# Performance work log

Hardware: AMD Instinct MI355X
Metric: run time of the kernel (lower is better)

The kernel has to match this reference:

```python
import jax, jax.numpy as jnp
import numpy as np

SIZE = 1024      # codebook entries
CODE_DIM = 256   # embedding dim


def setup_inputs() -> dict:
    key = jax.random.key(0)
    k_z, k_w = jax.random.split(key)
    z = jax.random.normal(k_z, (8, CODE_DIM, 16, 32, 32), dtype=jnp.float32)
    # init.uniform_(weight, -1/size, 1/size)
    codebook = jax.random.uniform(
        k_w, (SIZE, CODE_DIM), dtype=jnp.float32,
        minval=-1.0 / SIZE, maxval=1.0 / SIZE)
    return {"z": z, "codebook": codebook}


def reference(z, codebook):
    bs, d, t, h, w = z.shape
    # tokens: [N, d] with N = bs*t*h*w (matches permute(0,2,3,4,1).reshape(-1,d))
    zf = jnp.transpose(z, (0, 2, 3, 4, 1)).reshape(-1, d)
    # squared-distance expansion instead of materializing [size, N, d]:
    # ||z - e||^2 = ||z||^2 - 2 z.e + ||e||^2 ; argmin identical to argmin of norm
    d2 = (jnp.sum(zf * zf, axis=1, keepdims=True)
          - 2.0 * (zf @ codebook.T)
          + jnp.sum(codebook * codebook, axis=1))  # [N, size]
    encoding_indices = jnp.argmin(d2, axis=-1).reshape(bs, t, h, w)
    # gather + permute back to [bs, d, t, h, w]
    quantized = jnp.transpose(codebook[encoding_indices], (0, 4, 1, 2, 3))
    st = z + jax.lax.stop_gradient(quantized - z)  # straight-through output
    return (quantized, st, encoding_indices)
```

## Files before the change

### kernel.cpp

```cpp
#include <hip/hip_runtime.h>
#include <stdint.h>


constexpr int Dd  = 256;
constexpr int SPB = 16384;
constexpr int Nn  = 131072;
constexpr int Kk  = 1024;
constexpr int CCAP = 16;
#define WWIN 2.2e-3f

typedef short short8 __attribute__((ext_vector_type(8)));
typedef float v4f    __attribute__((ext_vector_type(4)));

__device__ __forceinline__ unsigned bf16pk(float a, float b){
  unsigned ua = __float_as_uint(a), ub = __float_as_uint(b);
  ua = (ua + 0x7fffu + ((ua >> 16) & 1u)) >> 16;
  ub = (ub + 0x7fffu + ((ub >> 16) & 1u)) & 0xffff0000u;
  return ua | ub;
}
__device__ __forceinline__ short8 frg(uint4 u){
  union { uint4 a; short8 b; } x; x.a = u; return x.b;
}
__device__ __forceinline__ v4f mfma16(short8 a, short8 b, v4f c){
  return __builtin_amdgcn_mfma_f32_16x16x32_bf16(a, b, c, 0, 0, 0);
}
__device__ __forceinline__ void dma16(const void* g, void* l){
  __builtin_amdgcn_global_load_lds((const __attribute__((address_space(1))) void*)g,
                                   (__attribute__((address_space(3))) void*)l, 16, 0, 0);
}

__global__ __launch_bounds__(64) void cnorm_k(const float* __restrict__ cb,
                                              float* __restrict__ cn){
  const int k = blockIdx.x, l = threadIdx.x;
  const float* row = cb + (size_t)k * Dd;
  float s = 0.f;
  #pragma unroll
  for (int c = 0; c < Dd; c += 64){ float v = row[c + l]; s += v * v; }
  #pragma unroll
  for (int off = 32; off > 0; off >>= 1) s += __shfl_down(s, off, 64);
  if (l == 0) cn[k] = s;
}

__global__ __launch_bounds__(256) void cconv_k(const float* __restrict__ cb,
                                               uint4* __restrict__ Bg){
  const int cc = blockIdx.x, n = threadIdx.x;
  const float* row = cb + (size_t)(cc * 256 + n) * Dd;
  for (int dc = 0; dc < 8; dc++){
    float v[32];
    const float4* rp = (const float4*)(row + dc * 32);
    #pragma unroll
    for (int q = 0; q < 8; q++){
      float4 f = rp[q]; v[4*q]=f.x; v[4*q+1]=f.y; v[4*q+2]=f.z; v[4*q+3]=f.w;
    }
    unsigned hv[16];
    #pragma unroll
    for (int p = 0; p < 16; p++) hv[p] = bf16pk(v[2*p], v[2*p+1]);
    size_t base = ((size_t)cc * 8 + dc) * 1024;
    #pragma unroll
    for (int kq = 0; kq < 4; kq++)
      Bg[base + (size_t)kq*256 + n] = make_uint4(hv[4*kq],hv[4*kq+1],hv[4*kq+2],hv[4*kq+3]);
  }
}

__global__ __launch_bounds__(256) void zconv_k(const float* __restrict__ z,
                                               uint4* __restrict__ Ag){
  const int tid = threadIdx.x, blk = blockIdx.x;
  const int b = blk >> 7, sb = (blk & 127) * 128;
  const int m = tid & 127, kqh = tid >> 7;
  const float* zb = z + (size_t)b * Dd * SPB + sb + m;
  for (int dc = 0; dc < 8; dc++){
    float v[16];
    #pragma unroll
    for (int s = 0; s < 16; s++) v[s] = zb[(size_t)(dc*32 + kqh*16 + s) * SPB];
    unsigned hv[8];
    #pragma unroll
    for (int p = 0; p < 8; p++) hv[p] = bf16pk(v[2*p], v[2*p+1]);
    size_t base = ((size_t)blk * 8 + dc) * 512;
    Ag[base + (size_t)(kqh*2+0)*128 + m] = make_uint4(hv[0],hv[1],hv[2],hv[3]);
    Ag[base + (size_t)(kqh*2+1)*128 + m] = make_uint4(hv[4],hv[5],hv[6],hv[7]);
  }
}

__global__ __launch_bounds__(512) void vq_sweep_k(const uint4* __restrict__ Ag,
                                                  const uint4* __restrict__ Bg,
                                                  const float* __restrict__ cnG,
                                                  int* __restrict__ cntW,
                                                  unsigned short* __restrict__ candW,
                                                  int* __restrict__ abestW){
  __shared__ uint4 AswF[2][2048];
  __shared__ uint4 BswF[2][2048];
  __shared__ unsigned bestP[256];
  __shared__ int cnt[256];
  __shared__ uint4 candU[256][2];
  unsigned short* cand = (unsigned short*)candU;

  const int tid = threadIdx.x, bId = blockIdx.x;
  const int w = tid >> 6, ln = tid & 63;
  const int li = ln & 15, lq = ln >> 4;
  const int wm = w >> 2, wn = w & 3;

  if (tid < 256){ bestP[tid] = 0xFFFFFFFFu; cnt[tid] = 0; }

  float cnr[4][4];
  #pragma unroll
  for (int cc = 0; cc < 4; cc++)
    #pragma unroll
    for (int ni = 0; ni < 4; ni++)
      cnr[cc][ni] = cnG[cc*256 + wn*64 + ni*16 + li];

  int aOff[4], bOff[4];
  #pragma unroll
  for (int c = 0; c < 4; c++){
    const int f = c*512 + w*64 + ln;
    const int dcL = f >> 10, kq = (f >> 8) & 3, mn = f & 255;
    aOff[c] = ((2*bId + (mn >> 7))*8 + dcL)*512 + kq*128 + (mn & 127);
    bOff[c] = dcL*1024 + kq*256 + mn;
  }

  #pragma unroll
  for (int c = 0; c < 4; c++) dma16(Ag + aOff[c], &AswF[0][c*512 + w*64]);
  #pragma unroll
  for (int c = 0; c < 4; c++) dma16(Bg + bOff[c], &BswF[0][c*512 + w*64]);

  v4f acc[8][4];
  #pragma unroll
  for (int cc = 0; cc < 4; cc++){
    const v4f vz = {0.f, 0.f, 0.f, 0.f};
    #pragma unroll
    for (int mi = 0; mi < 8; mi++)
      #pragma unroll
      for (int ni = 0; ni < 4; ni++) acc[mi][ni] = vz;

    #pragma unroll
    for (int ksq = 0; ksq < 4; ksq++){
      const int ks = cc*4 + ksq;
      if (ks < 15){
        const int ksn = ks + 1, bufn = ksn & 1, kqn = ksn & 3;
        #pragma unroll
        for (int c = 0; c < 4; c++)
          dma16(Ag + aOff[c] + kqn*1024, &AswF[bufn][c*512 + w*64]);
        #pragma unroll
        for (int c = 0; c < 4; c++)
          dma16(Bg + bOff[c] + ksn*2048, &BswF[bufn][c*512 + w*64]);
        asm volatile("s_waitcnt vmcnt(8)" ::: "memory");
      } else {
        asm volatile("s_waitcnt vmcnt(0)" ::: "memory");
      }
      __builtin_amdgcn_s_barrier();
      asm volatile("" ::: "memory");

      const int buf = ks & 1;
      #pragma unroll
      for (int dcL = 0; dcL < 2; dcL++){
        const uint4* Ab = &AswF[buf][dcL*1024 + lq*256 + wm*128 + li];
        const uint4* Bb = &BswF[buf][dcL*1024 + lq*256 + wn*64  + li];
        uint4 b0 = Bb[0], b1 = Bb[16], b2 = Bb[32], b3 = Bb[48];
        __builtin_amdgcn_s_setprio(1);
        #pragma unroll
        for (int mi = 0; mi < 8; mi++){
          uint4 av = Ab[mi*16];
          acc[mi][0] = mfma16(frg(av), frg(b0), acc[mi][0]);
          acc[mi][1] = mfma16(frg(av), frg(b1), acc[mi][1]);
          acc[mi][2] = mfma16(frg(av), frg(b2), acc[mi][2]);
          acc[mi][3] = mfma16(frg(av), frg(b3), acc[mi][3]);
        }
        __builtin_amdgcn_s_setprio(0);
      }
      asm volatile("s_waitcnt lgkmcnt(0)" ::: "memory");
      __builtin_amdgcn_s_barrier();
      asm volatile("" ::: "memory");
    }

    const int codeB = cc*256 + wn*64 + li;
    #pragma unroll
    for (int mi = 0; mi < 8; mi++){
      #pragma unroll
      for (int r = 0; r < 4; r++){
        unsigned pm = 0xFFFFFFFFu;
        #pragma unroll
        for (int ni = 0; ni < 4; ni++){
          float s = fmaf(acc[mi][ni][r], -2.0f, cnr[cc][ni]);
          unsigned u = __float_as_uint(s);
          u ^= (unsigned)((int)u >> 31) | 0x80000000u;
          unsigned p = (u & 0xFFFFFC00u) | (unsigned)(codeB + ni*16);
          acc[mi][ni][r] = __uint_as_float(p);
          pm = (pm < p) ? pm : p;
        }
        #pragma unroll
        for (int off = 1; off < 16; off <<= 1){
          unsigned o = (unsigned)__shfl_xor((int)pm, off, 16);
          pm = (pm < o) ? pm : o;
        }
        if (li == 0) atomicMin(&bestP[wm*128 + mi*16 + lq*4 + r], pm);
      }
    }
    asm volatile("s_waitcnt lgkmcnt(0)" ::: "memory");
    __builtin_amdgcn_s_barrier();
    asm volatile("" ::: "memory");
    #pragma unroll
    for (int mi = 0; mi < 8; mi++){
      #pragma unroll
      for (int r = 0; r < 4; r++){
        const int row = wm*128 + mi*16 + lq*4 + r;
        unsigned bp = bestP[row] & 0xFFFFFC00u;
        unsigned fb = (bp & 0x80000000u) ? (bp ^ 0x80000000u) : ~bp;
        float thr = __uint_as_float(fb) + WWIN;
        unsigned tu = __float_as_uint(thr);
        tu ^= (unsigned)((int)tu >> 31) | 0x80000000u;
        tu |= 1023u;
        #pragma unroll
        for (int ni = 0; ni < 4; ni++){
          unsigned p = __float_as_uint(acc[mi][ni][r]);
          if (p <= tu){
            int pos = atomicAdd(&cnt[row], 1);
            if (pos < CCAP) cand[row*CCAP + pos] = (unsigned short)(p & 1023u);
          }
        }
      }
    }
  }

  asm volatile("s_waitcnt lgkmcnt(0)" ::: "memory");
  __builtin_amdgcn_s_barrier();
  asm volatile("" ::: "memory");
  if (tid < 256){
    const int tok = bId*256 + tid;
    cntW[tok] = cnt[tid];
    abestW[tok] = (int)(bestP[tid] & 1023u);
    uint4* dst = (uint4*)&candW[(size_t)tok * CCAP];
    dst[0] = candU[tid][0];
    dst[1] = candU[tid][1];
  }
}

__global__ __launch_bounds__(256) void vq_rescore_k(const float* __restrict__ z,
                                                    const float* __restrict__ cb,
                                                    const float* __restrict__ cnG,
                                                    const int* __restrict__ cntW,
                                                    const unsigned short* __restrict__ candW,
                                                    const int* __restrict__ abestW,
                                                    int* __restrict__ idsW,
                                                    float* __restrict__ out){
  const int tok = blockIdx.x * 256 + threadIdx.x;
  const int b = tok >> 14, s = tok & 16383;
  const float* zr = z + (size_t)b * Dd * SPB + s;

  int n = cntW[tok];
  const bool ovf = (n > CCAP);
  if (ovf) n = CCAP;
  unsigned short cds[CCAP];
  *(uint4*)&cds[0] = *(const uint4*)&candW[(size_t)tok * CCAP];
  *(uint4*)&cds[8] = *(const uint4*)&candW[(size_t)tok * CCAP + 8];

  float bv = 3.4e38f; int bi = 0x7fffffff;
  float znl = 0.f;
  const int ngroups = (n + 3) >> 2;
  const int total = ovf ? ngroups + 1 : ngroups;

  for (int g = 0; g < total; g++){
    int idxs[4];
    #pragma unroll
    for (int ss = 0; ss < 4; ss++){
      int slot = g*4 + ss; if (slot >= n) slot = n - 1;
      idxs[ss] = (g < ngroups) ? (int)cds[slot] : abestW[tok];
    }
    const float* cr0 = cb + (size_t)idxs[0] * Dd;
    const float* cr1 = cb + (size_t)idxs[1] * Dd;
    const float* cr2 = cb + (size_t)idxs[2] * Dd;
    const float* cr3 = cb + (size_t)idxs[3] * Dd;
    float a0=0.f, a1=0.f, a2=0.f, a3=0.f, za=0.f;
    for (int d = 0; d < Dd; d += 8){
      float zv[8];
      #pragma unroll
      for (int j = 0; j < 8; j++) zv[j] = zr[(size_t)(d + j) * SPB];
      float4 c0a = *(const float4*)(cr0 + d), c0b = *(const float4*)(cr0 + d + 4);
      float4 c1a = *(const float4*)(cr1 + d), c1b = *(const float4*)(cr1 + d + 4);
      float4 c2a = *(const float4*)(cr2 + d), c2b = *(const float4*)(cr2 + d + 4);
      float4 c3a = *(const float4*)(cr3 + d), c3b = *(const float4*)(cr3 + d + 4);
      float cv0[8] = {c0a.x,c0a.y,c0a.z,c0a.w,c0b.x,c0b.y,c0b.z,c0b.w};
      float cv1[8] = {c1a.x,c1a.y,c1a.z,c1a.w,c1b.x,c1b.y,c1b.z,c1b.w};
      float cv2[8] = {c2a.x,c2a.y,c2a.z,c2a.w,c2b.x,c2b.y,c2b.z,c2b.w};
      float cv3[8] = {c3a.x,c3a.y,c3a.z,c3a.w,c3b.x,c3b.y,c3b.z,c3b.w};
      #pragma unroll
      for (int j = 0; j < 8; j++){
        if (g == 0) za = fmaf(zv[j], zv[j], za);
        a0 = fmaf(zv[j], cv0[j], a0);
        a1 = fmaf(zv[j], cv1[j], a1);
        a2 = fmaf(zv[j], cv2[j], a2);
        a3 = fmaf(zv[j], cv3[j], a3);
      }
    }
    if (g == 0) znl = za;
    float av[4] = {a0, a1, a2, a3};
    const int lim = (g < ngroups) ? n : 1;
    #pragma unroll
    for (int ss = 0; ss < 4; ss++){
      if (g*4 + ss < lim || (g >= ngroups && ss == 0)){
        float t  = znl - 2.0f * av[ss];
        float d2 = t + cnG[idxs[ss]];
        if (d2 < bv || (d2 == bv && idxs[ss] < bi)){ bv = d2; bi = idxs[ss]; }
      }
    }
  }
  idsW[tok] = bi;
  out[(size_t)2 * Nn * Dd + tok] = (float)bi;
}

__global__ __launch_bounds__(256) void vq_gather_k(const float* __restrict__ cb,
                                                   const int* __restrict__ idsW,
                                                   float* __restrict__ out){
  __shared__ float tile[64][129];
  __shared__ int lid[64];
  const int tid = threadIdx.x, blk = blockIdx.x;
  const int b = blk >> 8, s0 = (blk & 255) * 64;
  if (tid < 64) lid[tid] = idsW[b * SPB + s0 + tid];
  __syncthreads();

  const int r2 = tid >> 7, c = tid & 127;
  const int s = tid & 63, cq = tid >> 6;
  float* qb  = out + (size_t)b * Dd * SPB + s0 + s;
  float* stb = qb + (size_t)Nn * Dd;

  for (int ch = 0; ch < 2; ch++){
    #pragma unroll 4
    for (int t0 = 0; t0 < 64; t0 += 2){
      const int row = t0 + r2;
      tile[row][c] = cb[(size_t)lid[row] * Dd + ch*128 + c];
    }
    __syncthreads();
    #pragma unroll 8
    for (int i = 0; i < 32; i++){
      const int cc2 = i*4 + cq;
      const float v = tile[s][cc2];
      const size_t off = (size_t)(ch*128 + cc2) * SPB;
      qb[off]  = v;
      stb[off] = v;
    }
    __syncthreads();
  }
}

#define MICRO_STEP(WITH_ZN)                                                    \
    {                                                                          \
        float4 a0 = *(const float4*)&As[d][ty * 8];                            \
        float4 a1 = *(const float4*)&As[d][ty * 8 + 4];                        \
        float4 b0 = *(const float4*)&Bs[d][tx * 8];                            \
        float4 b1 = *(const float4*)&Bs[d][tx * 8 + 4];                        \
        float a[8] = {a0.x, a0.y, a0.z, a0.w, a1.x, a1.y, a1.z, a1.w};         \
        float bb[8] = {b0.x, b0.y, b0.z, b0.w, b1.x, b1.y, b1.z, b1.w};        \
        _Pragma("unroll")                                                      \
        for (int i = 0; i < 8; i++) {                                          \
            _Pragma("unroll")                                                  \
            for (int j = 0; j < 8; j++) acc[i][j] += a[i] * bb[j];             \
            if (WITH_ZN) zn[i] += a[i] * a[i];                                 \
        }                                                                      \
    }

__global__ __launch_bounds__(256) void vq_k(const float* __restrict__ z,
                                            const float* __restrict__ cb,
                                            const float* __restrict__ cn,
                                            float* __restrict__ out){
  __shared__ float As[16][128];
  __shared__ float Bs[16][132];
  __shared__ int   idsf[128];
  const int tid = threadIdx.x;
  const int tx = tid & 15, ty = tid >> 4;
  const int blk = blockIdx.x;
  const int b = blk >> 7, sb = (blk & 127) * 128;
  const float* zb = z + (size_t)b * Dd * SPB + sb;
  float bestv[8]; int besti[8]; float zn[8];
  #pragma unroll
  for (int i = 0; i < 8; i++){ bestv[i] = 3.4e38f; besti[i] = 0; zn[i] = 0.f; }
  const int am = tid & 127, ad = tid >> 7;
  const int bd = tid & 15,  bk = tid >> 4;
  for (int cc = 0; cc < 8; cc++){
    float acc[8][8];
    #pragma unroll
    for (int i = 0; i < 8; i++)
      #pragma unroll
      for (int j = 0; j < 8; j++) acc[i][j] = 0.f;
    for (int dc = 0; dc < 16; dc++){
      #pragma unroll
      for (int r = 0; r < 8; r++){
        const int d = ad + r * 2;
        As[d][am] = zb[(size_t)(dc*16 + d) * SPB + am];
      }
      #pragma unroll
      for (int r = 0; r < 8; r++){
        const int k = bk + r * 16;
        Bs[bd][k] = cb[(size_t)(cc*128 + k) * Dd + dc*16 + bd];
      }
      __syncthreads();
      if (cc == 0){
        #pragma unroll
        for (int d = 0; d < 16; d++) MICRO_STEP(1)
      } else {
        #pragma unroll
        for (int d = 0; d < 16; d++) MICRO_STEP(0)
      }
      __syncthreads();
    }
    const float* cnp = cn + cc*128 + tx*8;
    float4 c0 = *(const float4*)cnp;
    float4 c1 = *(const float4*)(cnp + 4);
    float cv[8] = {c0.x, c0.y, c0.z, c0.w, c1.x, c1.y, c1.z, c1.w};
    #pragma unroll
    for (int i = 0; i < 8; i++){
      #pragma unroll
      for (int j = 0; j < 8; j++){
        float t  = zn[i] - 2.0f * acc[i][j];
        float d2 = t + cv[j];
        int   ix = cc*128 + tx*8 + j;
        if (d2 < bestv[i]){ bestv[i] = d2; besti[i] = ix; }
      }
    }
  }
  #pragma unroll
  for (int i = 0; i < 8; i++){
    float v = bestv[i]; int ix = besti[i];
    #pragma unroll
    for (int off = 8; off > 0; off >>= 1){
      float ov = __shfl_down(v, off, 16);
      int   oi = __shfl_down(ix, off, 16);
      if (ov < v || (ov == v && oi < ix)){ v = ov; ix = oi; }
    }
    if (tx == 0) idsf[ty*8 + i] = ix;
  }
  __syncthreads();
  if (tid < 128) out[(size_t)2*Nn*Dd + (size_t)blk*128 + tid] = (float)idsf[tid];
  const int m = tid & 127, cg = tid >> 7;
  const int myidx = idsf[m];
  const float* crow = cb + (size_t)myidx * Dd + cg*128;
  float* q  = out + (size_t)b * Dd * SPB + (size_t)cg * 128 * SPB + sb + m;
  float* st = q + (size_t)Nn * Dd;
  #pragma unroll 8
  for (int r = 0; r < 128; r++){
    const float v = crow[r];
    q[(size_t)r * SPB]  = v;
    st[(size_t)r * SPB] = v;
  }
}

extern "C" void kernel_launch(void* const* d_in, const int* in_sizes, int n_in,
                              void* d_out, int out_size, void* d_ws, size_t ws_size,
                              hipStream_t stream){
  const float* z  = (const float*)d_in[0];
  const float* cb = (const float*)d_in[1];
  float* out = (float*)d_out;

  const size_t AG_B  = (size_t)1024 * 8 * 512 * 16;
  const size_t BG_B  = (size_t)4 * 8 * 1024 * 16;
  const size_t CN_B  = (size_t)Kk * 4;
  const size_t CNT_B = (size_t)Nn * 4;
  const size_t CAN_B = (size_t)Nn * CCAP * 2;
  const size_t ABW_B = (size_t)Nn * 4;
  const size_t IDS_B = (size_t)Nn * 4;
  const size_t NEED = AG_B + BG_B + CN_B + CNT_B + CAN_B + ABW_B + IDS_B;

  if (ws_size >= NEED){
    uint8_t* ws = (uint8_t*)d_ws;
    size_t o = 0;
    uint4* Ag   = (uint4*)(ws + o);          o += AG_B;
    uint4* Bg   = (uint4*)(ws + o);          o += BG_B;
    float* cnG  = (float*)(ws + o);          o += CN_B;
    int*   cntW = (int*)(ws + o);            o += CNT_B;
    unsigned short* candW = (unsigned short*)(ws + o); o += CAN_B;
    int*   abW  = (int*)(ws + o);            o += ABW_B;
    int*   idsW = (int*)(ws + o);            o += IDS_B;

    cnorm_k<<<Kk, 64, 0, stream>>>(cb, cnG);
    cconv_k<<<4, 256, 0, stream>>>(cb, Bg);
    zconv_k<<<Nn/128, 256, 0, stream>>>(z, Ag);
    vq_sweep_k<<<Nn/256, 512, 0, stream>>>(Ag, Bg, cnG, cntW, candW, abW);
    vq_rescore_k<<<Nn/256, 256, 0, stream>>>(z, cb, cnG, cntW, candW, abW, idsW, out);
    vq_gather_k<<<Nn/64, 256, 0, stream>>>(cb, idsW, out);
  } else {
    float* cn = (float*)d_ws;
    cnorm_k<<<Kk, 64, 0, stream>>>(cb, cn);
    vq_k<<<Nn/128, 256, 0, stream>>>(z, cb, cn, out);
  }
}
```

Before: 724.4 us.

## Fuse z bf16 conversion into sweep, keep A in registers, stream codebook chunks

Removes the separate zconv kernel and its Ag workspace. The sweep kernel now loads z directly, converts it to bf16 and holds the A fragments in registers for the whole sweep. It loops over 64-code codebook chunks with double-buffered LDS. Per-row best and candidate tracking move from LDS atomics to registers plus wave ballots, with candidates written straight to global memory. This saves one kernel launch and the Ag global write and reread, but the z loads are strided, the running threshold tightens progressively so more candidates may be recorded, and register pressure is higher.

```diff
diff --git a/kernel.cpp b/kernel.cpp
--- a/kernel.cpp
+++ b/kernel.cpp
@@ -62,174 +62,162 @@
   }
 }
 
-__global__ __launch_bounds__(256) void zconv_k(const float* __restrict__ z,
-                                               uint4* __restrict__ Ag){
-  const int tid = threadIdx.x, blk = blockIdx.x;
-  const int b = blk >> 7, sb = (blk & 127) * 128;
-  const int m = tid & 127, kqh = tid >> 7;
-  const float* zb = z + (size_t)b * Dd * SPB + sb + m;
-  for (int dc = 0; dc < 8; dc++){
-    float v[16];
-    #pragma unroll
-    for (int s = 0; s < 16; s++) v[s] = zb[(size_t)(dc*32 + kqh*16 + s) * SPB];
-    unsigned hv[8];
-    #pragma unroll
-    for (int p = 0; p < 8; p++) hv[p] = bf16pk(v[2*p], v[2*p+1]);
-    size_t base = ((size_t)blk * 8 + dc) * 512;
-    Ag[base + (size_t)(kqh*2+0)*128 + m] = make_uint4(hv[0],hv[1],hv[2],hv[3]);
-    Ag[base + (size_t)(kqh*2+1)*128 + m] = make_uint4(hv[4],hv[5],hv[6],hv[7]);
-  }
-}
-
-__global__ __launch_bounds__(512) void vq_sweep_k(const uint4* __restrict__ Ag,
-                                                  const uint4* __restrict__ Bg,
-                                                  const float* __restrict__ cnG,
-                                                  int* __restrict__ cntW,
-                                                  unsigned short* __restrict__ candW,
-                                                  int* __restrict__ abestW){
-  __shared__ uint4 AswF[2][2048];
-  __shared__ uint4 BswF[2][2048];
-  __shared__ unsigned bestP[256];
-  __shared__ int cnt[256];
-  __shared__ uint4 candU[256][2];
-  unsigned short* cand = (unsigned short*)candU;
+__global__ __launch_bounds__(512, 4) void vq_sweep_k(const float* __restrict__ z,
+                                                     const uint4* __restrict__ Bg,
+                                                     const float* __restrict__ cnG,
+                                                     int* __restrict__ cntW,
+                                                     unsigned short* __restrict__ candW,
+                                                     int* __restrict__ abestW){
+  __shared__ uint4 Bs[2][2048];
+  __shared__ float cnS[1024];
 
   const int tid = threadIdx.x, bId = blockIdx.x;
   const int w = tid >> 6, ln = tid & 63;
   const int li = ln & 15, lq = ln >> 4;
-  const int wm = w >> 2, wn = w & 3;
-
-  if (tid < 256){ bestP[tid] = 0xFFFFFFFFu; cnt[tid] = 0; }
-
-  float cnr[4][4];
-  #pragma unroll
-  for (int cc = 0; cc < 4; cc++)
-    #pragma unroll
-    for (int ni = 0; ni < 4; ni++)
-      cnr[cc][ni] = cnG[cc*256 + wn*64 + ni*16 + li];
-
-  int aOff[4], bOff[4];
-  #pragma unroll
-  for (int c = 0; c < 4; c++){
-    const int f = c*512 + w*64 + ln;
-    const int dcL = f >> 10, kq = (f >> 8) & 3, mn = f & 255;
-    aOff[c] = ((2*bId + (mn >> 7))*8 + dcL)*512 + kq*128 + (mn & 127);
-    bOff[c] = dcL*1024 + kq*256 + mn;
-  }
-
-  #pragma unroll
-  for (int c = 0; c < 4; c++) dma16(Ag + aOff[c], &AswF[0][c*512 + w*64]);
-  #pragma unroll
-  for (int c = 0; c < 4; c++) dma16(Bg + bOff[c], &BswF[0][c*512 + w*64]);
-
-  v4f acc[8][4];
-  #pragma unroll
-  for (int cc = 0; cc < 4; cc++){
+
+  const int tok0 = bId * 256;
+  const int b = tok0 >> 14;
+  const int s0 = tok0 & 16383;
+  const float* zb = z + (size_t)b * Dd * SPB + s0;
+  short8 aF[2][8];
+  #pragma unroll
+  for (int mi = 0; mi < 2; mi++){
+    const int tl = w*32 + mi*16 + li;
+    #pragma unroll
+    for (int kk = 0; kk < 8; kk++){
+      float v[8];
+      #pragma unroll
+      for (int j = 0; j < 8; j++)
+        v[j] = zb[(size_t)(kk*32 + lq*8 + j) * SPB + tl];
+      union { unsigned u[4]; short8 s8; } x;
+      #pragma unroll
+      for (int p = 0; p < 4; p++) x.u[p] = bf16pk(v[2*p], v[2*p+1]);
+      aF[mi][kk] = x.s8;
+    }
+  }
+
+  if (w < 4) dma16((const uint4*)cnG + w*64 + ln, (uint4*)&cnS[w*256]);
+  int bOff[4];
+  #pragma unroll
+  for (int j = 0; j < 4; j++){
+    const int f = j*512 + tid;
+    bOff[j] = (f >> 8)*1024 + ((f >> 6) & 3)*256 + (f & 63);
+  }
+  #pragma unroll
+  for (int j = 0; j < 4; j++)
+    dma16(Bg + bOff[j], &Bs[0][j*512 + w*64]);
+
+  unsigned bestR[8]; int cntR[8];
+  #pragma unroll
+  for (int i = 0; i < 8; i++){ bestR[i] = 0xFFFFFFFFu; cntR[i] = 0; }
+
+  for (int c = 0; c < 16; c++){
+    if (c < 15){
+      const int cn1 = c + 1;
+      const size_t srcB = (size_t)(cn1 >> 2)*8192 + (size_t)((cn1 & 3)*64);
+      uint4* dstB = &Bs[cn1 & 1][0];
+      #pragma unroll
+      for (int j = 0; j < 4; j++)
+        dma16(Bg + srcB + bOff[j], dstB + j*512 + w*64);
+      asm volatile("s_waitcnt vmcnt(4)" ::: "memory");
+    } else {
+      asm volatile("s_waitcnt vmcnt(0)" ::: "memory");
+    }
+    __builtin_amdgcn_s_barrier();
+    asm volatile("" ::: "memory");
+
+    v4f acc[2][4];
     const v4f vz = {0.f, 0.f, 0.f, 0.f};
     #pragma unroll
-    for (int mi = 0; mi < 8; mi++)
+    for (int mi = 0; mi < 2; mi++)
       #pragma unroll
       for (int ni = 0; ni < 4; ni++) acc[mi][ni] = vz;
 
-    #pragma unroll
-    for (int ksq = 0; ksq < 4; ksq++){
-      const int ks = cc*4 + ksq;
-      if (ks < 15){
-        const int ksn = ks + 1, bufn = ksn & 1, kqn = ksn & 3;
-        #pragma unroll
-        for (int c = 0; c < 4; c++)
-          dma16(Ag + aOff[c] + kqn*1024, &AswF[bufn][c*512 + w*64]);
-        #pragma unroll
-        for (int c = 0; c < 4; c++)
-          dma16(Bg + bOff[c] + ksn*2048, &BswF[bufn][c*512 + w*64]);
-        asm volatile("s_waitcnt vmcnt(8)" ::: "memory");
-      } else {
-        asm volatile("s_waitcnt vmcnt(0)" ::: "memory");
-      }
-      __builtin_amdgcn_s_barrier();
-      asm volatile("" ::: "memory");
-
-      const int buf = ks & 1;
-      #pragma unroll
-      for (int dcL = 0; dcL < 2; dcL++){
-        const uint4* Ab = &AswF[buf][dcL*1024 + lq*256 + wm*128 + li];
-        const uint4* Bb = &BswF[buf][dcL*1024 + lq*256 + wn*64  + li];
-        uint4 b0 = Bb[0], b1 = Bb[16], b2 = Bb[32], b3 = Bb[48];
-        __builtin_amdgcn_s_setprio(1);
-        #pragma unroll
-        for (int mi = 0; mi < 8; mi++){
-          uint4 av = Ab[mi*16];
-          acc[mi][0] = mfma16(frg(av), frg(b0), acc[mi][0]);
-          acc[mi][1] = mfma16(frg(av), frg(b1), acc[mi][1]);
-          acc[mi][2] = mfma16(frg(av), frg(b2), acc[mi][2]);
-          acc[mi][3] = mfma16(frg(av), frg(b3), acc[mi][3]);
-        }
-        __builtin_amdgcn_s_setprio(0);
-      }
-      asm volatile("s_waitcnt lgkmcnt(0)" ::: "memory");
-      __builtin_amdgcn_s_barrier();
-      asm volatile("" ::: "memory");
-    }
-
-    const int codeB = cc*256 + wn*64 + li;
-    #pragma unroll
-    for (int mi = 0; mi < 8; mi++){
+    const uint4* Bbase = &Bs[c & 1][lq*64 + li];
+    __builtin_amdgcn_s_setprio(1);
+    #pragma unroll
+    for (int kk = 0; kk < 8; kk++){
+      short8 b0 = frg(Bbase[kk*256 +  0]);
+      short8 b1 = frg(Bbase[kk*256 + 16]);
+      short8 b2 = frg(Bbase[kk*256 + 32]);
+      short8 b3 = frg(Bbase[kk*256 + 48]);
+      #pragma unroll
+      for (int mi = 0; mi < 2; mi++){
+        acc[mi][0] = mfma16(aF[mi][kk], b0, acc[mi][0]);
+        acc[mi][1] = mfma16(aF[mi][kk], b1, acc[mi][1]);
+        acc[mi][2] = mfma16(aF[mi][kk], b2, acc[mi][2]);
+        acc[mi][3] = mfma16(aF[mi][kk], b3, acc[mi][3]);
+      }
+    }
+    __builtin_amdgcn_s_setprio(0);
+
+    float cnv[4];
+    #pragma unroll
+    for (int ni = 0; ni < 4; ni++) cnv[ni] = cnS[c*64 + ni*16 + li];
+
+    const int codeB = c*64 + li;
+    #pragma unroll
+    for (int mi = 0; mi < 2; mi++){
       #pragma unroll
       for (int r = 0; r < 4; r++){
+        const int i = mi*4 + r;
         unsigned pm = 0xFFFFFFFFu;
         #pragma unroll
         for (int ni = 0; ni < 4; ni++){
-          float s = fmaf(acc[mi][ni][r], -2.0f, cnr[cc][ni]);
+          float s = fmaf(acc[mi][ni][r], -2.0f, cnv[ni]);
           unsigned u = __float_as_uint(s);
           u ^= (unsigned)((int)u >> 31) | 0x80000000u;
           unsigned p = (u & 0xFFFFFC00u) | (unsigned)(codeB + ni*16);
           acc[mi][ni][r] = __uint_as_float(p);
           pm = (pm < p) ? pm : p;
         }
+        unsigned pmw = pm;
         #pragma unroll
         for (int off = 1; off < 16; off <<= 1){
-          unsigned o = (unsigned)__shfl_xor((int)pm, off, 16);
-          pm = (pm < o) ? pm : o;
+          unsigned o = (unsigned)__shfl_xor((int)pmw, off, 16);
+          pmw = (pmw < o) ? pmw : o;
         }
-        if (li == 0) atomicMin(&bestP[wm*128 + mi*16 + lq*4 + r], pm);
-      }
-    }
-    asm volatile("s_waitcnt lgkmcnt(0)" ::: "memory");
+        bestR[i] = (bestR[i] < pmw) ? bestR[i] : pmw;
+        unsigned bp = bestR[i] & 0xFFFFFC00u;
+        unsigned fb = (bp & 0x80000000u) ? (bp ^ 0x80000000u) : ~bp;
+        float thrf = __uint_as_float(fb) + WWIN;
+        unsigned tu = __float_as_uint(thrf);
+        tu ^= (unsigned)((int)tu >> 31) | 0x80000000u;
+        tu |= 1023u;
+        if (__any(pm <= tu)){
+          const int tok = tok0 + w*32 + mi*16 + lq*4 + r;
+          int base = cntR[i];
+          #pragma unroll
+          for (int ni = 0; ni < 4; ni++){
+            const unsigned p = __float_as_uint(acc[mi][ni][r]);
+            const bool pass = (p <= tu);
+            unsigned long long bal = __ballot(pass);
+            const unsigned bq = (unsigned)(bal >> (lq*16)) & 0xFFFFu;
+            if (pass){
+              int pos = base + __popc(bq & ((1u << li) - 1u));
+              if (pos < CCAP)
+                candW[(size_t)tok*CCAP + pos] = (unsigned short)(p & 1023u);
+            }
+            base += __popc(bq);
+          }
+          cntR[i] = base;
+        }
+      }
+    }
     __builtin_amdgcn_s_barrier();
     asm volatile("" ::: "memory");
-    #pragma unroll
-    for (int mi = 0; mi < 8; mi++){
+  }
+
+  if (li == 0){
+    #pragma unroll
+    for (int mi = 0; mi < 2; mi++)
       #pragma unroll
       for (int r = 0; r < 4; r++){
-        const int row = wm*128 + mi*16 + lq*4 + r;
-        unsigned bp = bestP[row] & 0xFFFFFC00u;
-        unsigned fb = (bp & 0x80000000u) ? (bp ^ 0x80000000u) : ~bp;
-        float thr = __uint_as_float(fb) + WWIN;
-        unsigned tu = __float_as_uint(thr);
-        tu ^= (unsigned)((int)tu >> 31) | 0x80000000u;
-        tu |= 1023u;
-        #pragma unroll
-        for (int ni = 0; ni < 4; ni++){
-          unsigned p = __float_as_uint(acc[mi][ni][r]);
-          if (p <= tu){
-            int pos = atomicAdd(&cnt[row], 1);
-            if (pos < CCAP) cand[row*CCAP + pos] = (unsigned short)(p & 1023u);
-          }
-        }
-      }
-    }
-  }
-
-  asm volatile("s_waitcnt lgkmcnt(0)" ::: "memory");
-  __builtin_amdgcn_s_barrier();
-  asm volatile("" ::: "memory");
-  if (tid < 256){
-    const int tok = bId*256 + tid;
-    cntW[tok] = cnt[tid];
-    abestW[tok] = (int)(bestP[tid] & 1023u);
-    uint4* dst = (uint4*)&candW[(size_t)tok * CCAP];
-    dst[0] = candU[tid][0];
-    dst[1] = candU[tid][1];
+        const int i = mi*4 + r;
+        const int tok = tok0 + w*32 + mi*16 + lq*4 + r;
+        cntW[tok] = cntR[i];
+        abestW[tok] = (int)(bestR[i] & 1023u);
+      }
   }
 }
 
@@ -448,19 +436,17 @@
   const float* cb = (const float*)d_in[1];
   float* out = (float*)d_out;
 
-  const size_t AG_B  = (size_t)1024 * 8 * 512 * 16;
   const size_t BG_B  = (size_t)4 * 8 * 1024 * 16;
   const size_t CN_B  = (size_t)Kk * 4;
   const size_t CNT_B = (size_t)Nn * 4;
   const size_t CAN_B = (size_t)Nn * CCAP * 2;
   const size_t ABW_B = (size_t)Nn * 4;
   const size_t IDS_B = (size_t)Nn * 4;
-  const size_t NEED = AG_B + BG_B + CN_B + CNT_B + CAN_B + ABW_B + IDS_B;
+  const size_t NEED = BG_B + CN_B + CNT_B + CAN_B + ABW_B + IDS_B;
 
   if (ws_size >= NEED){
     uint8_t* ws = (uint8_t*)d_ws;
     size_t o = 0;
-    uint4* Ag   = (uint4*)(ws + o);          o += AG_B;
     uint4* Bg   = (uint4*)(ws + o);          o += BG_B;
     float* cnG  = (float*)(ws + o);          o += CN_B;
     int*   cntW = (int*)(ws + o);            o += CNT_B;
@@ -470,8 +456,7 @@
 
     cnorm_k<<<Kk, 64, 0, stream>>>(cb, cnG);
     cconv_k<<<4, 256, 0, stream>>>(cb, Bg);
-    zconv_k<<<Nn/128, 256, 0, stream>>>(z, Ag);
-    vq_sweep_k<<<Nn/256, 512, 0, stream>>>(Ag, Bg, cnG, cntW, candW, abW);
+    vq_sweep_k<<<Nn/256, 512, 0, stream>>>(z, Bg, cnG, cntW, candW, abW);
     vq_rescore_k<<<Nn/256, 256, 0, stream>>>(z, cb, cnG, cntW, candW, abW, idsW, out);
     vq_gather_k<<<Nn/64, 256, 0, stream>>>(cb, idsW, out);
   } else {
```

Result: no change. 717.7 us (-0.9%).
